# Performance work log

Hardware: AMD Instinct MI355X
Metric: run time of the kernel (lower is better)

Reference implementation:

```python
import jax, jax.numpy as jnp
import numpy as np

B, S, D, H = 1, 4096, 768, 12
HID = 3072
HD = D // H  # 64
EPS = 1e-5


def _layer_norm(x, w, b):
    mean = jnp.mean(x, axis=-1, keepdims=True)
    var = jnp.mean(jnp.square(x - mean), axis=-1, keepdims=True)  # unbiased=False
    return w * ((x - mean) / jnp.sqrt(var + EPS)) + b


def setup_inputs() -> dict:
    key = jax.random.key(0)
    ks = jax.random.split(key, 8)
    s_d = 1.0 / np.sqrt(D)
    s_h = 1.0 / np.sqrt(HID)
    return {
        "x": jax.random.normal(ks[0], (B, S, D), dtype=jnp.float32),
        "Wqkv": jax.random.normal(ks[1], (D, 3 * D), dtype=jnp.float32) * s_d,
        "bqkv": jnp.zeros((3 * D,), dtype=jnp.float32),
        "Wo": jax.random.normal(ks[2], (D, D), dtype=jnp.float32) * s_d,
        "bo": jnp.zeros((D,), dtype=jnp.float32),
        "ln1_w": jnp.ones((D,), dtype=jnp.float32),
        "ln1_b": jnp.zeros((D,), dtype=jnp.float32),
        "W1": jax.random.normal(ks[3], (D, HID), dtype=jnp.float32) * s_d,
        "b1": jnp.zeros((HID,), dtype=jnp.float32),
        "W2": jax.random.normal(ks[4], (HID, D), dtype=jnp.float32) * s_h,
        "b2": jnp.zeros((D,), dtype=jnp.float32),
        "ln2_w": jnp.ones((D,), dtype=jnp.float32),
        "ln2_b": jnp.zeros((D,), dtype=jnp.float32),
    }


def reference(x, Wqkv, bqkv, Wo, bo, ln1_w, ln1_b, W1, b1, W2, b2, ln2_w, ln2_b):
    b, s, d = x.shape
    # --- multi-head self-attention (naive: full [B,H,S,S] scores) ---
    qkv = x @ Wqkv + bqkv                              # [B,S,3D]
    q, k, v = jnp.split(qkv, 3, axis=-1)
    split = lambda t: t.reshape(b, s, H, HD).transpose(0, 2, 1, 3)  # [B,H,S,hd]
    q, k, v = split(q), split(k), split(v)
    scores = jnp.einsum("bhqd,bhkd->bhqk", q, k) / jnp.sqrt(jnp.float32(HD))
    attn_w = jax.nn.softmax(scores, axis=-1)           # [B,H,S,S]
    h = jnp.einsum("bhqk,bhkd->bhqd", attn_w, v)
    h = h.transpose(0, 2, 1, 3).reshape(b, s, d)       # merge heads
    attn_out = h @ Wo + bo
    # --- post-norm residual 1 ---
    x1 = _layer_norm(x + attn_out, ln1_w, ln1_b)
    # --- FFN ---
    ff = jax.nn.gelu(x1 @ W1 + b1, approximate=False) @ W2 + b2
    # --- post-norm residual 2 ---
    return _layer_norm(x1 + ff, ln2_w, ln2_b)
```

## Files before the change

kernel.cpp:

```cpp
#include <hip/hip_runtime.h>
#include <hip/hip_bf16.h>

typedef __attribute__((ext_vector_type(8))) short bf16x8;
typedef __attribute__((ext_vector_type(4))) short short4v;
typedef __attribute__((ext_vector_type(4))) float f32x4;
typedef __attribute__((ext_vector_type(16))) float f32x16;
typedef __attribute__((ext_vector_type(4))) unsigned int uint4v;

__device__ inline unsigned short f2b(float f){
  unsigned int u = __float_as_uint(f);
  unsigned int r = (u + 0x7fffu + ((u >> 16) & 1u)) >> 16;
  return (unsigned short)r;
}
__device__ inline float b2f(unsigned short u){
  return __uint_as_float(((unsigned int)u) << 16);
}
__device__ inline unsigned int pk_fast(float lo, float hi){
  return ((__float_as_uint(hi) + 0x8000u) & 0xffff0000u)
       | ((__float_as_uint(lo) + 0x8000u) >> 16);
}
__device__ inline float pair_sum(float x){
  return x + __shfl_xor(x, 32);
}
__device__ inline float gelu_tanh(float x){
  float x3 = x*x*x;
  float y = 0.79788456080286536f*x + 0.035677408136300125f*x3;
  float a = fminf(y * 2.8853900817779268f, 80.f);
  float t = __builtin_amdgcn_exp2f(a);
  return x * t * __builtin_amdgcn_rcpf(t + 1.f);
}

__global__ __launch_bounds__(256) void prep_kernel(
    const float* __restrict__ Wqkv, short* __restrict__ WqkvT,
    const float* __restrict__ Wo,   short* __restrict__ WoT,
    const float* __restrict__ W1,   short* __restrict__ W1T,
    const float* __restrict__ W2,   short* __restrict__ W2T,
    const float* __restrict__ x,    short* __restrict__ xb){
  __shared__ float tile[32][33];
  const int b = blockIdx.x;
  const float* A; short* AT; int R, C, bx, by;
  if (b < 1728){ A=Wqkv; AT=WqkvT; R=768;  C=2304; bx=b%72;        by=b/72; }
  else if (b < 2304){ int c=b-1728; A=Wo; AT=WoT; R=768;  C=768;  bx=c%24; by=c/24; }
  else if (b < 4608){ int c=b-2304; A=W1; AT=W1T; R=768;  C=3072; bx=c%96; by=c/96; }
  else if (b < 6912){ int c=b-4608; A=W2; AT=W2T; R=3072; C=768;  bx=c%24; by=c/24; }
  else {
    int i = (b - 6912)*256 + threadIdx.x;
    float4 v = reinterpret_cast<const float4*>(x)[i];
    short4v o;
    o[0] = (short)f2b(v.x); o[1] = (short)f2b(v.y);
    o[2] = (short)f2b(v.z); o[3] = (short)f2b(v.w);
    reinterpret_cast<short4v*>(xb)[i] = o;
    return;
  }
  const int tx = threadIdx.x & 31, ty = threadIdx.x >> 5;
  const int c0 = bx*32, r0 = by*32;
  #pragma unroll
  for (int i = 0; i < 4; i++)
    tile[ty + i*8][tx] = A[(size_t)(r0 + ty + i*8)*C + c0 + tx];
  __syncthreads();
  #pragma unroll
  for (int i = 0; i < 4; i++){
    int c = c0 + ty + i*8, r = r0 + tx;
    AT[(size_t)c*R + r] = (short)f2b(tile[tx][ty + i*8]);
  }
}

template<int OUTMODE, int RESID, int GELU>
__global__ __launch_bounds__(256) void gemm_kernel(
    const short* __restrict__ A, const short* __restrict__ BT,
    const float* __restrict__ bias, const float* __restrict__ resid,
    float* __restrict__ outF, short* __restrict__ outB, short* __restrict__ outB2,
    short* __restrict__ outB3,
    int M, int N, int K, int G, int cpr, int byc)
{
  __shared__ short As[3][128*32];
  __shared__ short Bs[3][128*32];
  const int xcd = blockIdx.x & 7, r = blockIdx.x >> 3;
  const int bx = (xcd % cpr)*G + (r % G);
  const int by = (xcd / cpr)*byc + (r / G);
  const int m0 = by * 128, n0 = bx * 128;

  const int lane = threadIdx.x & 63, wid = threadIdx.x >> 6;
  const int l15 = lane & 15, l4 = lane >> 4;
  const int wr = wid >> 1, wc = wid & 1;

  f32x4 acc[4][4];
  #pragma unroll
  for (int i = 0; i < 4; i++)
    #pragma unroll
    for (int j = 0; j < 4; j++) acc[i][j] = (f32x4){0.f,0.f,0.f,0.f};

  const int arow = wid*16 + (lane >> 2);
  const int sswz = (((lane & 3) ^ ((lane >> 3) & 3))) * 8;
  const short* Ag = A  + (size_t)(m0 + arow)*K + sswz;
  const short* Bg = BT + (size_t)(n0 + arow)*K + sswz;

  const int NT = K >> 5;

  auto STAGE = [&](int buf, int k0){
    #pragma unroll
    for (int p = 0; p < 2; p++){
      __builtin_amdgcn_global_load_lds(
          (const __attribute__((address_space(1))) void*)(Ag + (size_t)p*64*K + k0),
          (__attribute__((address_space(3))) void*)(&As[buf][(p*64 + wid*16)*32]), 16, 0, 0);
      __builtin_amdgcn_global_load_lds(
          (const __attribute__((address_space(1))) void*)(Bg + (size_t)p*64*K + k0),
          (__attribute__((address_space(3))) void*)(&Bs[buf][(p*64 + wid*16)*32]), 16, 0, 0);
    }
  };

  STAGE(0, 0);
  STAGE(1, 32);

  const int rchunk = (l15 >> 1) & 3;
  int cur = 0;
  for (int t = 0; t < NT; t++){
    if (t + 1 < NT) asm volatile("s_waitcnt vmcnt(4)" ::: "memory");
    else            asm volatile("s_waitcnt vmcnt(0)" ::: "memory");
    __builtin_amdgcn_s_barrier();
    __builtin_amdgcn_sched_barrier(0);
    const short* as = &As[cur][0];
    const short* bs = &Bs[cur][0];
    bf16x8 av[4], bv[4];
    #pragma unroll
    for (int i = 0; i < 4; i++)
      av[i] = *(const bf16x8*)(as + (wr*64 + i*16 + l15)*32 + ((l4 ^ rchunk) * 8));
    #pragma unroll
    for (int i = 0; i < 4; i++)
      bv[i] = *(const bf16x8*)(bs + (wc*64 + i*16 + l15)*32 + ((l4 ^ rchunk) * 8));
    #pragma unroll
    for (int i = 0; i < 4; i++)
      #pragma unroll
      for (int j = 0; j < 4; j++)
        acc[i][j] = __builtin_amdgcn_mfma_f32_16x16x32_bf16(av[i], bv[j], acc[i][j], 0, 0, 0);
    if (t + 2 < NT){
      int s2 = cur + 2; if (s2 >= 3) s2 -= 3;
      STAGE(s2, (t + 2) << 5);
    }
    cur = (cur == 2) ? 0 : cur + 1;
  }

  if constexpr (OUTMODE == 2){
    const float SCQ = 0.125f * 1.44269504088896341f;
    #pragma unroll
    for (int i = 0; i < 4; i++){
      const int row0 = m0 + wr*64 + i*16 + l4*4;
      const size_t rQK = (size_t)(row0>>5)*2048 + (size_t)(row0&31)*8;
      const size_t rV  = (size_t)(row0>>5)*2048 + (size_t)((row0>>4)&1)*1024
                       + (size_t)((row0>>3)&1)*256 + (size_t)(row0&7);
      #pragma unroll
      for (int j = 0; j < 4; j++){
        const int col = n0 + wc*64 + j*16 + l15;
        const float bval = bias[col];
        if (col < 1536){
          const int isQ = (col < 768);
          const float qs = isQ ? SCQ : 1.f;
          const int c2 = isQ ? col : (col - 768);
          short* dst = isQ ? outB : outB2;
          const int head = c2 >> 6, dh = c2 & 63;
          const size_t base = (size_t)head*262144 + (size_t)(dh>>4)*512
                            + (size_t)((dh>>3)&1)*256 + (size_t)(dh&7) + rQK;
          dst[base]      = (short)f2b((acc[i][j][0] + bval) * qs);
          dst[base + 8]  = (short)f2b((acc[i][j][1] + bval) * qs);
          dst[base + 16] = (short)f2b((acc[i][j][2] + bval) * qs);
          dst[base + 24] = (short)f2b((acc[i][j][3] + bval) * qs);
        } else {
          const int c2 = col - 1536;
          const int head = c2 >> 6, dh = c2 & 63;
          const size_t base = (size_t)head*262144 + (size_t)(dh>>5)*512
                            + (size_t)(dh&31)*8 + rV;
          short4v sv;
          sv[0] = (short)f2b(acc[i][j][0] + bval);
          sv[1] = (short)f2b(acc[i][j][1] + bval);
          sv[2] = (short)f2b(acc[i][j][2] + bval);
          sv[3] = (short)f2b(acc[i][j][3] + bval);
          *(short4v*)(outB3 + base) = sv;
        }
      }
    }
  } else {
    #pragma unroll
    for (int i = 0; i < 4; i++){
      const int row0 = m0 + wr*64 + i*16 + l4*4;
      #pragma unroll
      for (int j = 0; j < 4; j++){
        const int col = n0 + wc*64 + j*16 + l15;
        const float bval = bias[col];
        #pragma unroll
        for (int jj = 0; jj < 4; jj++){
          const int row = row0 + jj;
          float v = acc[i][j][jj] + bval;
          if constexpr (RESID) v += resid[(size_t)row*N + col];
          if constexpr (GELU)  v = gelu_tanh(v);
          if constexpr (OUTMODE == 0){
            outF[(size_t)row*N + col] = v;
          } else {
            outB[(size_t)row*N + col] = (short)f2b(v);
          }
        }
      }
    }
  }
}

__global__ __launch_bounds__(256) void attn8_kernel(
    const short* __restrict__ Qf, const short* __restrict__ Kf,
    const short* __restrict__ Vf, short* __restrict__ hout){
  __shared__ float Ols[4][32][33];
  __shared__ float Lls[4][32];
  const int g = (blockIdx.x & 7) * 192 + (blockIdx.x >> 3);
  const int head = g >> 7;
  const int qt = g & 127;
  const int lane = threadIdx.x & 63, w = threadIdx.x >> 6;
  const int l31 = lane & 31, hi = lane >> 5;

  bf16x8 qf0, qf1, qf2, qf3;
  {
    const short* qp = Qf + (size_t)(head*128 + qt)*2048 + lane*8;
    qf0 = *(const bf16x8*)(qp);
    qf1 = *(const bf16x8*)(qp + 512);
    qf2 = *(const bf16x8*)(qp + 1024);
    qf3 = *(const bf16x8*)(qp + 1536);
  }

  float l_run = 0.f;
  f32x16 o0, o1;
  #pragma unroll
  for (int r = 0; r < 16; r++){ o0[r] = 0.f; o1[r] = 0.f; }

  const short* kp0 = Kf + (size_t)(head*128 + w*32)*2048 + lane*8;
  const short* vp0 = Vf + (size_t)(head*128 + w*32)*2048 + lane*8;

  auto PROC = [&](bf16x8 k0, bf16x8 k1, bf16x8 k2, bf16x8 k3, int t){
    const short* vp = vp0 + t*2048;
    bf16x8 v00 = *(const bf16x8*)(vp);
    bf16x8 v01 = *(const bf16x8*)(vp + 512);
    bf16x8 v10 = *(const bf16x8*)(vp + 1024);
    bf16x8 v11 = *(const bf16x8*)(vp + 1536);

    f32x16 s;
    #pragma unroll
    for (int r = 0; r < 16; r++) s[r] = 0.f;
    s = __builtin_amdgcn_mfma_f32_32x32x16_bf16(k0, qf0, s, 0, 0, 0);
    s = __builtin_amdgcn_mfma_f32_32x32x16_bf16(k1, qf1, s, 0, 0, 0);
    s = __builtin_amdgcn_mfma_f32_32x32x16_bf16(k2, qf2, s, 0, 0, 0);
    s = __builtin_amdgcn_mfma_f32_32x32x16_bf16(k3, qf3, s, 0, 0, 0);

    #pragma unroll
    for (int r = 0; r < 16; r++) s[r] = __builtin_amdgcn_exp2f(s[r]);
    float c0s = (s[0]+s[1]) + (s[2]+s[3]);
    float c1s = (s[4]+s[5]) + (s[6]+s[7]);
    float c2s = (s[8]+s[9]) + (s[10]+s[11]);
    float c3s = (s[12]+s[13]) + (s[14]+s[15]);
    l_run += pair_sum((c0s + c1s) + (c2s + c3s));

    unsigned int c01 = pk_fast(s[0],  s[1]),  c23 = pk_fast(s[2],  s[3]);
    unsigned int c45 = pk_fast(s[4],  s[5]),  c67 = pk_fast(s[6],  s[7]);
    unsigned int c89 = pk_fast(s[8],  s[9]),  cab = pk_fast(s[10], s[11]);
    unsigned int ccd = pk_fast(s[12], s[13]), cef = pk_fast(s[14], s[15]);
    unsigned int x01 = (unsigned int)__shfl_xor((int)c01, 32);
    unsigned int x23 = (unsigned int)__shfl_xor((int)c23, 32);
    unsigned int x45 = (unsigned int)__shfl_xor((int)c45, 32);
    unsigned int x67 = (unsigned int)__shfl_xor((int)c67, 32);
    unsigned int x89 = (unsigned int)__shfl_xor((int)c89, 32);
    unsigned int xab = (unsigned int)__shfl_xor((int)cab, 32);
    unsigned int xcd = (unsigned int)__shfl_xor((int)ccd, 32);
    unsigned int xef = (unsigned int)__shfl_xor((int)cef, 32);
    uint4v u0 = { hi ? x45 : c01, hi ? x67 : c23, hi ? c45 : x01, hi ? c67 : x23 };
    uint4v u1 = { hi ? xcd : c89, hi ? xef : cab, hi ? ccd : x89, hi ? cef : xab };
    bf16x8 pb0 = __builtin_bit_cast(bf16x8, u0);
    bf16x8 pb1 = __builtin_bit_cast(bf16x8, u1);

    o0 = __builtin_amdgcn_mfma_f32_32x32x16_bf16(v00, pb0, o0, 0, 0, 0);
    o0 = __builtin_amdgcn_mfma_f32_32x32x16_bf16(v10, pb1, o0, 0, 0, 0);
    o1 = __builtin_amdgcn_mfma_f32_32x32x16_bf16(v01, pb0, o1, 0, 0, 0);
    o1 = __builtin_amdgcn_mfma_f32_32x32x16_bf16(v11, pb1, o1, 0, 0, 0);
  };

  bf16x8 kA0 = *(const bf16x8*)(kp0);
  bf16x8 kA1 = *(const bf16x8*)(kp0 + 512);
  bf16x8 kA2 = *(const bf16x8*)(kp0 + 1024);
  bf16x8 kA3 = *(const bf16x8*)(kp0 + 1536);
  for (int t = 0; t < 32; t += 2){
    const short* kpB = kp0 + (t+1)*2048;
    bf16x8 kB0 = *(const bf16x8*)(kpB);
    bf16x8 kB1 = *(const bf16x8*)(kpB + 512);
    bf16x8 kB2 = *(const bf16x8*)(kpB + 1024);
    bf16x8 kB3 = *(const bf16x8*)(kpB + 1536);
    PROC(kA0, kA1, kA2, kA3, t);
    const short* kpA = kp0 + ((t+2 < 32) ? (t+2) : 31)*2048;
    kA0 = *(const bf16x8*)(kpA);
    kA1 = *(const bf16x8*)(kpA + 512);
    kA2 = *(const bf16x8*)(kpA + 1024);
    kA3 = *(const bf16x8*)(kpA + 1536);
    PROC(kB0, kB1, kB2, kB3, t+1);
  }

  if (hi == 0) Lls[w][l31] = l_run;
  #pragma unroll
  for (int r = 0; r < 16; r++){
    int d = (r & 3) + 8*(r >> 2) + 4*hi;
    Ols[w][l31][d] = o0[r];
  }
  __syncthreads();
  const int t = threadIdx.x;
  const int q = t >> 2, dc = (t & 3) * 8;
  float inv;
  if (t < 128){
    float l = Lls[0][q] + Lls[1][q] + Lls[2][q] + Lls[3][q];
    inv = 1.f / l;
    bf16x8 res;
    #pragma unroll
    for (int j = 0; j < 8; j++){
      float o = Ols[0][q][dc+j] + Ols[1][q][dc+j]
              + Ols[2][q][dc+j] + Ols[3][q][dc+j];
      res[j] = (short)f2b(o * inv);
    }
    *(bf16x8*)(hout + (size_t)(qt*32 + q)*768 + head*64 + dc) = res;
  }
  __syncthreads();
  #pragma unroll
  for (int r = 0; r < 16; r++){
    int d = (r & 3) + 8*(r >> 2) + 4*hi;
    Ols[w][l31][d] = o1[r];
  }
  __syncthreads();
  if (t < 128){
    bf16x8 res;
    #pragma unroll
    for (int j = 0; j < 8; j++){
      float o = Ols[0][q][dc+j] + Ols[1][q][dc+j]
              + Ols[2][q][dc+j] + Ols[3][q][dc+j];
      res[j] = (short)f2b(o * inv);
    }
    *(bf16x8*)(hout + (size_t)(qt*32 + q)*768 + head*64 + 32 + dc) = res;
  }
}

template<int WRITE_BF16>
__global__ __launch_bounds__(256) void ln_kernel(
    const float* __restrict__ in, const float* __restrict__ g, const float* __restrict__ b,
    float* __restrict__ outF, short* __restrict__ outB){
  const int row = blockIdx.x;
  const float* x = in + (size_t)row * 768;
  const int t = threadIdx.x;
  float v[3];
  #pragma unroll
  for (int i = 0; i < 3; i++) v[i] = x[t + i*256];
  float s  = v[0] + v[1] + v[2];
  float s2 = v[0]*v[0] + v[1]*v[1] + v[2]*v[2];
  #pragma unroll
  for (int off = 1; off < 64; off <<= 1){
    s  += __shfl_xor(s,  off);
    s2 += __shfl_xor(s2, off);
  }
  __shared__ float red[8];
  if ((t & 63) == 0){ red[t >> 6] = s; red[4 + (t >> 6)] = s2; }
  __syncthreads();
  s  = red[0] + red[1] + red[2] + red[3];
  s2 = red[4] + red[5] + red[6] + red[7];
  const float mean = s * (1.f/768.f);
  const float rstd = rsqrtf(s2*(1.f/768.f) - mean*mean + 1e-5f);
  #pragma unroll
  for (int i = 0; i < 3; i++){
    int c = t + i*256;
    float y = g[c] * ((v[i] - mean) * rstd) + b[c];
    outF[(size_t)row*768 + c] = y;
    if constexpr (WRITE_BF16) outB[(size_t)row*768 + c] = (short)f2b(y);
  }
}

extern "C" void kernel_launch(void* const* d_in, const int* in_sizes, int n_in,
                              void* d_out, int out_size, void* d_ws, size_t ws_size,
                              hipStream_t stream){
  const float* x    = (const float*)d_in[0];
  const float* Wqkv = (const float*)d_in[1];
  const float* bqkv = (const float*)d_in[2];
  const float* Wo   = (const float*)d_in[3];
  const float* bo   = (const float*)d_in[4];
  const float* ln1w = (const float*)d_in[5];
  const float* ln1b = (const float*)d_in[6];
  const float* W1   = (const float*)d_in[7];
  const float* b1   = (const float*)d_in[8];
  const float* W2   = (const float*)d_in[9];
  const float* b2   = (const float*)d_in[10];
  const float* ln2w = (const float*)d_in[11];
  const float* ln2b = (const float*)d_in[12];
  float* out = (float*)d_out;

  char* ws = (char*)d_ws;
  short* WqkvT = (short*)(ws + 0);
  short* WoT   = (short*)(ws + 3538944);
  short* W1T   = (short*)(ws + 4718592);
  short* W2T   = (short*)(ws + 9437184);
  short* xb    = (short*)(ws + 14155776);
  short* Qfb   = (short*)(ws + 20447232);
  short* Kfb   = (short*)(ws + 26738688);
  short* Vfb   = (short*)(ws + 33030144);
  short* hb    = (short*)(ws + 39321600);
  float* res1  = (float*)(ws + 45613056);
  float* x1f   = (float*)(ws + 58195968);
  short* x1b   = (short*)(ws + 70778880);
  short* h1b   = (short*)(ws + 77070336);
  float* y2 = res1;

  dim3 blk(256);
  prep_kernel<<<dim3(9984), blk, 0, stream>>>(
      Wqkv, WqkvT, Wo, WoT, W1, W1T, W2, W2T, x, xb);

  gemm_kernel<2,0,0><<<dim3(576), blk, 0, stream>>>(
      xb, WqkvT, bqkv, nullptr, nullptr, Qfb, Kfb, Vfb, 4096, 2304, 768, 9, 2, 8);
  attn8_kernel<<<dim3(1536), blk, 0, stream>>>(Qfb, Kfb, Vfb, hb);
  gemm_kernel<0,1,0><<<dim3(192), blk, 0, stream>>>(
      hb, WoT, bo, x, res1, nullptr, nullptr, nullptr, 4096, 768, 768, 6, 1, 4);
  ln_kernel<1><<<dim3(4096), blk, 0, stream>>>(res1, ln1w, ln1b, x1f, x1b);
  gemm_kernel<1,0,1><<<dim3(768), blk, 0, stream>>>(
      x1b, W1T, b1, nullptr, nullptr, h1b, nullptr, nullptr, 4096, 3072, 768, 12, 2, 8);
  gemm_kernel<0,1,0><<<dim3(192), blk, 0, stream>>>(
      h1b, W2T, b2, x1f, y2, nullptr, nullptr, nullptr, 4096, 768, 3072, 6, 1, 4);
  ln_kernel<0><<<dim3(4096), blk, 0, stream>>>(y2, ln2w, ln2b, out, nullptr);
}
```

Before: 226.1 us.

## Split-K the N=768 GEMMs into two partial planes, merging residual and bias in LayerNorm

The Wo and W2 GEMMs, which only had 192 tiles, now run with a 2-way K split over 384 blocks. Each split writes raw fp32 partials to its own plane. The LayerNorm kernel now sums the two planes, the residual and the bias before normalizing, which removes the epilogue residual read from the GEMMs. The goal is better CU occupancy on a 256-CU part. The cost is extra fp32 partial traffic, plus a per-block rotation of the K-tile start to spread memory access. The change also swaps rounding bf16 packing for truncation in attention, which slightly lowers accuracy.

New measurement: 214.8 us. 1.05x faster.

```diff
diff --git a/kernel.cpp b/kernel.cpp
--- a/kernel.cpp
+++ b/kernel.cpp
@@ -15,9 +15,8 @@
 __device__ inline float b2f(unsigned short u){
   return __uint_as_float(((unsigned int)u) << 16);
 }
-__device__ inline unsigned int pk_fast(float lo, float hi){
-  return ((__float_as_uint(hi) + 0x8000u) & 0xffff0000u)
-       | ((__float_as_uint(lo) + 0x8000u) >> 16);
+__device__ inline unsigned int pk_tr(float lo, float hi){
+  return (__float_as_uint(hi) & 0xffff0000u) | (__float_as_uint(lo) >> 16);
 }
 __device__ inline float pair_sum(float x){
   return x + __shfl_xor(x, 32);
@@ -65,17 +64,20 @@
   }
 }
 
-template<int OUTMODE, int RESID, int GELU>
+template<int OUTMODE, int GELU>
 __global__ __launch_bounds__(256) void gemm_kernel(
     const short* __restrict__ A, const short* __restrict__ BT,
-    const float* __restrict__ bias, const float* __restrict__ resid,
-    float* __restrict__ outF, short* __restrict__ outB, short* __restrict__ outB2,
-    short* __restrict__ outB3,
-    int M, int N, int K, int G, int cpr, int byc)
+    const float* __restrict__ bias,
+    float* __restrict__ outF, float* __restrict__ outF2,
+    short* __restrict__ outB, short* __restrict__ outB2, short* __restrict__ outB3,
+    int M, int N, int K, int ksplit, int nper, int G, int cpr, int byc)
 {
   __shared__ short As[3][128*32];
   __shared__ short Bs[3][128*32];
-  const int xcd = blockIdx.x & 7, r = blockIdx.x >> 3;
+  const int sb = blockIdx.x / nper;
+  const int b2 = blockIdx.x % nper;
+  const int kbase = sb * ksplit;
+  const int xcd = b2 & 7, r = b2 >> 3;
   const int bx = (xcd % cpr)*G + (r % G);
   const int by = (xcd / cpr)*byc + (r / G);
   const int m0 = by * 128, n0 = bx * 128;
@@ -95,7 +97,9 @@
   const short* Ag = A  + (size_t)(m0 + arow)*K + sswz;
   const short* Bg = BT + (size_t)(n0 + arow)*K + sswz;
 
-  const int NT = K >> 5;
+  const int NT = ksplit >> 5;
+  const int rot = b2 % NT;
+  auto kof = [&](int i){ int tt = i + rot; if (tt >= NT) tt -= NT; return kbase + (tt << 5); };
 
   auto STAGE = [&](int buf, int k0){
     #pragma unroll
@@ -109,8 +113,8 @@
     }
   };
 
-  STAGE(0, 0);
-  STAGE(1, 32);
+  STAGE(0, kof(0));
+  STAGE(1, kof(1));
 
   const int rchunk = (l15 >> 1) & 3;
   int cur = 0;
@@ -135,7 +139,7 @@
         acc[i][j] = __builtin_amdgcn_mfma_f32_16x16x32_bf16(av[i], bv[j], acc[i][j], 0, 0, 0);
     if (t + 2 < NT){
       int s2 = cur + 2; if (s2 >= 3) s2 -= 3;
-      STAGE(s2, (t + 2) << 5);
+      STAGE(s2, kof(t + 2));
     }
     cur = (cur == 2) ? 0 : cur + 1;
   }
@@ -178,6 +182,19 @@
         }
       }
     }
+  } else if constexpr (OUTMODE == 3){
+    float* dst = sb ? outF2 : outF;
+    #pragma unroll
+    for (int i = 0; i < 4; i++){
+      const int row0 = m0 + wr*64 + i*16 + l4*4;
+      #pragma unroll
+      for (int j = 0; j < 4; j++){
+        const int col = n0 + wc*64 + j*16 + l15;
+        #pragma unroll
+        for (int jj = 0; jj < 4; jj++)
+          dst[(size_t)(row0 + jj)*N + col] = acc[i][j][jj];
+      }
+    }
   } else {
     #pragma unroll
     for (int i = 0; i < 4; i++){
@@ -188,15 +205,9 @@
         const float bval = bias[col];
         #pragma unroll
         for (int jj = 0; jj < 4; jj++){
-          const int row = row0 + jj;
           float v = acc[i][j][jj] + bval;
-          if constexpr (RESID) v += resid[(size_t)row*N + col];
-          if constexpr (GELU)  v = gelu_tanh(v);
-          if constexpr (OUTMODE == 0){
-            outF[(size_t)row*N + col] = v;
-          } else {
-            outB[(size_t)row*N + col] = (short)f2b(v);
-          }
+          if constexpr (GELU) v = gelu_tanh(v);
+          outB[(size_t)(row0 + jj)*N + col] = (short)f2b(v);
         }
       }
     }
@@ -254,10 +265,10 @@
     float c3s = (s[12]+s[13]) + (s[14]+s[15]);
     l_run += pair_sum((c0s + c1s) + (c2s + c3s));
 
-    unsigned int c01 = pk_fast(s[0],  s[1]),  c23 = pk_fast(s[2],  s[3]);
-    unsigned int c45 = pk_fast(s[4],  s[5]),  c67 = pk_fast(s[6],  s[7]);
-    unsigned int c89 = pk_fast(s[8],  s[9]),  cab = pk_fast(s[10], s[11]);
-    unsigned int ccd = pk_fast(s[12], s[13]), cef = pk_fast(s[14], s[15]);
+    unsigned int c01 = pk_tr(s[0],  s[1]),  c23 = pk_tr(s[2],  s[3]);
+    unsigned int c45 = pk_tr(s[4],  s[5]),  c67 = pk_tr(s[6],  s[7]);
+    unsigned int c89 = pk_tr(s[8],  s[9]),  cab = pk_tr(s[10], s[11]);
+    unsigned int ccd = pk_tr(s[12], s[13]), cef = pk_tr(s[14], s[15]);
     unsigned int x01 = (unsigned int)__shfl_xor((int)c01, 32);
     unsigned int x23 = (unsigned int)__shfl_xor((int)c23, 32);
     unsigned int x45 = (unsigned int)__shfl_xor((int)c45, 32);
@@ -338,15 +349,20 @@
 }
 
 template<int WRITE_BF16>
-__global__ __launch_bounds__(256) void ln_kernel(
-    const float* __restrict__ in, const float* __restrict__ g, const float* __restrict__ b,
+__global__ __launch_bounds__(256) void ln_merge_kernel(
+    const float* __restrict__ p0, const float* __restrict__ p1,
+    const float* __restrict__ resid, const float* __restrict__ cbias,
+    const float* __restrict__ g, const float* __restrict__ b,
     float* __restrict__ outF, short* __restrict__ outB){
   const int row = blockIdx.x;
-  const float* x = in + (size_t)row * 768;
+  const size_t base = (size_t)row * 768;
   const int t = threadIdx.x;
   float v[3];
   #pragma unroll
-  for (int i = 0; i < 3; i++) v[i] = x[t + i*256];
+  for (int i = 0; i < 3; i++){
+    int c = t + i*256;
+    v[i] = p0[base + c] + p1[base + c] + resid[base + c] + cbias[c];
+  }
   float s  = v[0] + v[1] + v[2];
   float s2 = v[0]*v[0] + v[1]*v[1] + v[2]*v[2];
   #pragma unroll
@@ -365,8 +381,8 @@
   for (int i = 0; i < 3; i++){
     int c = t + i*256;
     float y = g[c] * ((v[i] - mean) * rstd) + b[c];
-    outF[(size_t)row*768 + c] = y;
-    if constexpr (WRITE_BF16) outB[(size_t)row*768 + c] = (short)f2b(y);
+    outF[base + c] = y;
+    if constexpr (WRITE_BF16) outB[base + c] = (short)f2b(y);
   }
 }
 
@@ -402,21 +418,29 @@
   float* x1f   = (float*)(ws + 58195968);
   short* x1b   = (short*)(ws + 70778880);
   short* h1b   = (short*)(ws + 77070336);
-  float* y2 = res1;
+  float* woP   = (float*)(ws + 77070336);
+  float* f2P1  = (float*)(ws + 20447232);
+  const int PLANE = 4096*768;
 
   dim3 blk(256);
   prep_kernel<<<dim3(9984), blk, 0, stream>>>(
       Wqkv, WqkvT, Wo, WoT, W1, W1T, W2, W2T, x, xb);
 
-  gemm_kernel<2,0,0><<<dim3(576), blk, 0, stream>>>(
-      xb, WqkvT, bqkv, nullptr, nullptr, Qfb, Kfb, Vfb, 4096, 2304, 768, 9, 2, 8);
+  gemm_kernel<2,0><<<dim3(576), blk, 0, stream>>>(
+      xb, WqkvT, bqkv, nullptr, nullptr, Qfb, Kfb, Vfb,
+      4096, 2304, 768, 768, 576, 9, 2, 8);
   attn8_kernel<<<dim3(1536), blk, 0, stream>>>(Qfb, Kfb, Vfb, hb);
-  gemm_kernel<0,1,0><<<dim3(192), blk, 0, stream>>>(
-      hb, WoT, bo, x, res1, nullptr, nullptr, nullptr, 4096, 768, 768, 6, 1, 4);
-  ln_kernel<1><<<dim3(4096), blk, 0, stream>>>(res1, ln1w, ln1b, x1f, x1b);
-  gemm_kernel<1,0,1><<<dim3(768), blk, 0, stream>>>(
-      x1b, W1T, b1, nullptr, nullptr, h1b, nullptr, nullptr, 4096, 3072, 768, 12, 2, 8);
-  gemm_kernel<0,1,0><<<dim3(192), blk, 0, stream>>>(
-      h1b, W2T, b2, x1f, y2, nullptr, nullptr, nullptr, 4096, 768, 3072, 6, 1, 4);
-  ln_kernel<0><<<dim3(4096), blk, 0, stream>>>(y2, ln2w, ln2b, out, nullptr);
-}
+  gemm_kernel<3,0><<<dim3(384), blk, 0, stream>>>(
+      hb, WoT, nullptr, woP, woP + PLANE, nullptr, nullptr, nullptr,
+      4096, 768, 768, 384, 192, 6, 1, 4);
+  ln_merge_kernel<1><<<dim3(4096), blk, 0, stream>>>(
+      woP, woP + PLANE, x, bo, ln1w, ln1b, x1f, x1b);
+  gemm_kernel<1,1><<<dim3(768), blk, 0, stream>>>(
+      x1b, W1T, b1, nullptr, nullptr, h1b, nullptr, nullptr,
+      4096, 3072, 768, 768, 768, 12, 2, 8);
+  gemm_kernel<3,0><<<dim3(384), blk, 0, stream>>>(
+      h1b, W2T, nullptr, res1, f2P1, nullptr, nullptr, nullptr,
+      4096, 768, 3072, 1536, 192, 6, 1, 4);
+  ln_merge_kernel<0><<<dim3(4096), blk, 0, stream>>>(
+      res1, f2P1, x1f, b2, ln2w, ln2b, out, nullptr);
+}
```
